# Kernel optimization log

Measured on AMD Instinct MI355X. Metric: run time of the kernel, lower is better.

## Reference

```python
import jax, jax.numpy as jnp
import numpy as np
from jax import lax

WINDOW_SIZE = 12
POOL = 4  # AvgPool2d(4): 12x12 -> 3x3

# 4 directional 3x3 kernels, stacked as [O=4, I=1, 3, 3]
_KERNELS = np.stack([
    np.array([[0, 0, 0], [-1, 1, 0], [0, 0, 0]], np.float32),  # left
    np.array([[0, 0, 0], [0, 1, -1], [0, 0, 0]], np.float32),  # right
    np.array([[0, -1, 0], [0, 1, 0], [0, 0, 0]], np.float32),  # up
    np.array([[0, 0, 0], [0, 1, 0], [0, -1, 0]], np.float32),  # down
])[:, None, :, :]


def setup_inputs() -> dict:
    key = jax.random.key(0)
    k1, k2 = jax.random.split(key)
    windows_num = 200000
    n = WINDOW_SIZE * WINDOW_SIZE * windows_num
    samples1 = jax.random.uniform(k1, (n, 3), dtype=jnp.float32)
    samples2 = jax.random.uniform(k2, (n, 3), dtype=jnp.float32)
    return {"samples1": samples1, "samples2": samples2, "windows_num": windows_num}


def _to_pooled(samples, windows_num):
    # [W*W*N, C] -> [W, W, N, C] -> [N, C, W, W]
    x = samples.reshape(WINDOW_SIZE, WINDOW_SIZE, windows_num, -1)
    x = jnp.transpose(x, (2, 3, 0, 1))
    # channel mean, keepdim -> [N, 1, W, W]
    m = jnp.mean(x, axis=1, keepdims=True)
    # AvgPool2d(4): [N,1,12,12] -> [N,1,3,3]
    hp = WINDOW_SIZE // POOL
    p = m.reshape(windows_num, 1, hp, POOL, hp, POOL).mean(axis=(3, 5))
    return p


def _dir_grads(x):
    # x: [N,1,3,3]; 4 directional 3x3 convs, padding=1 -> [N,4,3,3]
    k = jnp.asarray(_KERNELS)
    return lax.conv_general_dilated(
        x, k, window_strides=(1, 1), padding=[(1, 1), (1, 1)],
        dimension_numbers=("NCHW", "OIHW", "NCHW"))


def reference(samples1, samples2, windows_num):
    org_pool = _to_pooled(samples1, windows_num)
    enh_pool = _to_pooled(samples2, windows_num)
    d_org = _dir_grads(org_pool)
    d_enh = _dir_grads(enh_pool)
    # squared diff per direction, summed over the 4 directions -> [N,3,3]
    E = jnp.sum((d_org - d_enh) ** 2, axis=1)
    return jnp.mean(E)
```

## Files before the change

### kernel.cpp

```cpp
#include <hip/hip_runtime.h>

__global__ __launch_bounds__(512) void spa_kernel(
    const float* __restrict__ s1, const float* __restrict__ s2,
    float* __restrict__ out, int N, float scale) {
  const int win = blockIdx.x * 512 + threadIdx.x;

  float P[9];
#pragma unroll
  for (int k = 0; k < 9; ++k) P[k] = 0.f;

  if (win < N) {
    const size_t stride = (size_t)N * 3u;
    const float* p1 = s1 + (size_t)win * 3u;
    const float* p2 = s2 + (size_t)win * 3u;
#pragma unroll 1
    for (int i = 0; i < 12; ++i) {
      const int pr = (i >> 2) * 3;
#pragma unroll
      for (int j = 0; j < 12; ++j) {
        const float* a = p1 + (size_t)j * stride;
        const float* b = p2 + (size_t)j * stride;
        float d = (a[0] + a[1] + a[2]) - (b[0] + b[1] + b[2]);
        P[pr + (j >> 2)] += d;
      }
      p1 += (size_t)12 * stride;
      p2 += (size_t)12 * stride;
    }
  }

#pragma unroll
  for (int k = 0; k < 9; ++k) P[k] *= (1.0f / 48.0f);

  float e = 0.f;
#pragma unroll
  for (int i = 0; i < 3; ++i) {
#pragma unroll
    for (int j = 0; j < 3; ++j) {
      float c = P[i * 3 + j];
      float l = (j > 0) ? P[i * 3 + j - 1] : 0.f;
      float r = (j < 2) ? P[i * 3 + j + 1] : 0.f;
      float u = (i > 0) ? P[(i - 1) * 3 + j] : 0.f;
      float d = (i < 2) ? P[(i + 1) * 3 + j] : 0.f;
      float dl = c - l, dr = c - r, du = c - u, dd = c - d;
      e += dl * dl + dr * dr + du * du + dd * dd;
    }
  }

  const int lane = threadIdx.x & 63;
  const int wid = threadIdx.x >> 6;
#pragma unroll
  for (int off = 32; off > 0; off >>= 1) e += __shfl_down(e, off, 64);

  __shared__ float sPart[8];
  if (lane == 0) sPart[wid] = e;
  __syncthreads();
  if (threadIdx.x == 0) {
    float t = 0.f;
#pragma unroll
    for (int w = 0; w < 8; ++w) t += sPart[w];
    atomicAdd(out, t * scale);
  }
}

extern "C" void kernel_launch(void* const* d_in, const int* in_sizes, int n_in,
                              void* d_out, int out_size, void* d_ws, size_t ws_size,
                              hipStream_t stream) {
  const float* s1 = (const float*)d_in[0];
  const float* s2 = (const float*)d_in[1];
  float* out = (float*)d_out;
  int N = in_sizes[0] / (12 * 12 * 3);
  float scale = 1.0f / (9.0f * (float)N);
  hipMemsetAsync(d_out, 0, sizeof(float), stream);
  int blocks = (N + 511) / 512;
  spa_kernel<<<blocks, 512, 0, stream>>>(s1, s2, out, N, scale);
}
```

Baseline: 643.2 us.

## Process four windows per thread with 16-byte nontemporal vector loads

New measurement: 753.0 us. 17.1% more time.

```diff
diff --git a/kernel.cpp b/kernel.cpp
--- a/kernel.cpp
+++ b/kernel.cpp
@@ -1,10 +1,80 @@
 #include <hip/hip_runtime.h>
 
-__global__ __launch_bounds__(512) void spa_kernel(
+typedef float f32x4 __attribute__((ext_vector_type(4)));
+
+__global__ __launch_bounds__(64) void spa_kernel_v4(
+    const float* __restrict__ s1, const float* __restrict__ s2,
+    float* __restrict__ out, int N, float scale) {
+  const int g4 = blockIdx.x * 64 + (int)threadIdx.x;
+  const int nG = N >> 2;
+
+  float P[4][9];
+#pragma unroll
+  for (int w = 0; w < 4; ++w)
+#pragma unroll
+    for (int k = 0; k < 9; ++k) P[w][k] = 0.f;
+
+  if (g4 < nG) {
+    const size_t stride = (size_t)N * 3u;
+    const float* p1 = s1 + (size_t)g4 * 12u;
+    const float* p2 = s2 + (size_t)g4 * 12u;
+#pragma unroll 1
+    for (int i = 0; i < 12; ++i) {
+      const int pr = (i >> 2) * 3;
+#pragma unroll
+      for (int j = 0; j < 12; ++j) {
+        const f32x4* a = (const f32x4*)(p1 + (size_t)j * stride);
+        const f32x4* b = (const f32x4*)(p2 + (size_t)j * stride);
+        f32x4 a0 = __builtin_nontemporal_load(a);
+        f32x4 a1 = __builtin_nontemporal_load(a + 1);
+        f32x4 a2 = __builtin_nontemporal_load(a + 2);
+        f32x4 b0 = __builtin_nontemporal_load(b);
+        f32x4 b1 = __builtin_nontemporal_load(b + 1);
+        f32x4 b2 = __builtin_nontemporal_load(b + 2);
+        float d0 = (a0.x + a0.y + a0.z) - (b0.x + b0.y + b0.z);
+        float d1 = (a0.w + a1.x + a1.y) - (b0.w + b1.x + b1.y);
+        float d2 = (a1.z + a1.w + a2.x) - (b1.z + b1.w + b2.x);
+        float d3 = (a2.y + a2.z + a2.w) - (b2.y + b2.z + b2.w);
+        const int pc = pr + (j >> 2);
+        P[0][pc] += d0;
+        P[1][pc] += d1;
+        P[2][pc] += d2;
+        P[3][pc] += d3;
+      }
+      p1 += (size_t)12 * stride;
+      p2 += (size_t)12 * stride;
+    }
+  }
+
+  float e = 0.f;
+#pragma unroll
+  for (int w = 0; w < 4; ++w) {
+    float Q[9];
+#pragma unroll
+    for (int k = 0; k < 9; ++k) Q[k] = P[w][k] * (1.0f / 48.0f);
+#pragma unroll
+    for (int i = 0; i < 3; ++i)
+#pragma unroll
+      for (int j = 0; j < 3; ++j) {
+        float c = Q[i * 3 + j];
+        float l = (j > 0) ? Q[i * 3 + j - 1] : 0.f;
+        float r = (j < 2) ? Q[i * 3 + j + 1] : 0.f;
+        float u = (i > 0) ? Q[(i - 1) * 3 + j] : 0.f;
+        float d = (i < 2) ? Q[(i + 1) * 3 + j] : 0.f;
+        float dl = c - l, dr = c - r, du = c - u, dd = c - d;
+        e += dl * dl + dr * dr + du * du + dd * dd;
+      }
+  }
+
+#pragma unroll
+  for (int off = 32; off > 0; off >>= 1) e += __shfl_down(e, off, 64);
+  if ((threadIdx.x & 63) == 0) atomicAdd(out, e * scale);
+}
+
+__global__ __launch_bounds__(512) void spa_kernel_s(
     const float* __restrict__ s1, const float* __restrict__ s2,
     float* __restrict__ out, int N, float scale) {
   const int win = blockIdx.x * 512 + threadIdx.x;
-
   float P[9];
 #pragma unroll
   for (int k = 0; k < 9; ++k) P[k] = 0.f;
@@ -33,7 +103,7 @@
 
   float e = 0.f;
 #pragma unroll
-  for (int i = 0; i < 3; ++i) {
+  for (int i = 0; i < 3; ++i)
 #pragma unroll
     for (int j = 0; j < 3; ++j) {
       float c = P[i * 3 + j];
@@ -44,7 +114,6 @@
       float dl = c - l, dr = c - r, du = c - u, dd = c - d;
       e += dl * dl + dr * dr + du * du + dd * dd;
     }
-  }
 
   const int lane = threadIdx.x & 63;
   const int wid = threadIdx.x >> 6;
@@ -71,6 +140,12 @@
   int N = in_sizes[0] / (12 * 12 * 3);
   float scale = 1.0f / (9.0f * (float)N);
   hipMemsetAsync(d_out, 0, sizeof(float), stream);
-  int blocks = (N + 511) / 512;
-  spa_kernel<<<blocks, 512, 0, stream>>>(s1, s2, out, N, scale);
+  if ((N & 3) == 0) {
+    int nG = N >> 2;
+    int blocks = (nG + 63) / 64;
+    spa_kernel_v4<<<blocks, 64, 0, stream>>>(s1, s2, out, N, scale);
+  } else {
+    int blocks = (N + 511) / 512;
+    spa_kernel_s<<<blocks, 512, 0, stream>>>(s1, s2, out, N, scale);
+  }
 }
```
